# Kernel optimization log

Hardware: AMD Instinct MI355X
Metric: run time of the kernel (lower is better)

## Reference

```python
import jax, jax.numpy as jnp
import numpy as np

B, S, DIM, NH = 256, 64, 1024, 8
DH = DIM // NH
EPS = 1e-6
LN_EPS = 1e-5


def _make_hops(n):
    hops = np.zeros((n, n), dtype=np.int64)
    cur = 1
    for i in range(n):
        for j in range(i + 1, n):
            hops[i, j] = cur
            hops[j, i] = cur
            cur += 1
    return hops, cur


def setup_inputs() -> dict:
    key = jax.random.key(0)
    ks = jax.random.split(key, 8)
    hops_np, curnum = _make_hops(S)
    return {
        "q": jax.random.normal(ks[0], (B, S, DIM), dtype=jnp.float32),
        "k": jax.random.normal(ks[1], (B, S, DIM), dtype=jnp.float32),
        "v": jax.random.normal(ks[2], (B, S, DIM), dtype=jnp.float32),
        "igate_w": jax.random.normal(ks[3], (NH, 3 * DIM), dtype=jnp.float32) * 0.02,
        "igate_b": jax.random.normal(ks[4], (NH,), dtype=jnp.float32) * 0.1,
        "fgate_w": jax.random.normal(ks[5], (NH, 3 * DIM), dtype=jnp.float32) * 0.02,
        "fgate_b": jnp.linspace(3.0, 6.0, NH, dtype=jnp.float32),
        "rpe": jax.random.normal(ks[6], (curnum, DIM), dtype=jnp.float32) * 0.02,
        "ln_w": jax.random.normal(ks[7], (DIM,), dtype=jnp.float32) * 0.1,
        "ln_b": jnp.zeros((DIM,), dtype=jnp.float32),
        "hops": jnp.asarray(hops_np),
    }


def _mlstm_forward(q, k, v, igate_w, igate_b, fgate_w, fgate_b, rpe, ln_w, ln_b, hops):
    Bq, Sq, _ = q.shape
    pos_emb = rpe[hops]                                   # (S, S, DIM)
    gate_in = jnp.concatenate([q, k, v], axis=-1)         # (B, S, 3*DIM)
    ig = gate_in @ igate_w.T + igate_b                    # (B, S, NH)
    fg = gate_in @ fgate_w.T + fgate_b                    # (B, S, NH)
    ig = jnp.transpose(ig, (0, 2, 1))                     # (B, NH, S)
    fg = jnp.transpose(fg, (0, 2, 1))                     # (B, NH, S)

    qh = q.reshape(Bq, Sq, NH, DH).transpose(0, 2, 1, 3)  # (B, NH, S, DH)
    kh = k.reshape(Bq, Sq, NH, DH).transpose(0, 2, 1, 3)
    vh = v.reshape(Bq, Sq, NH, DH).transpose(0, 2, 1, 3)

    # log forget gates, cumulative sum with a leading zero
    log_f = jax.nn.log_sigmoid(fg)                        # (B, NH, S)
    csum = jnp.cumsum(log_f, axis=-1)
    csum = jnp.concatenate([jnp.zeros((Bq, NH, 1), csum.dtype), csum], axis=-1)  # (B,NH,S+1)
    lfm = csum[:, :, :, None] - csum[:, :, None, :]       # (B, NH, S+1, S+1)
    ltr = jnp.tril(jnp.ones((Sq, Sq), dtype=bool))
    log_fg_matrix = jnp.where(ltr, lfm[:, :, 1:, 1:], -jnp.inf)  # (B, NH, S, S)

    log_D = log_fg_matrix + ig[:, :, None, :]             # add i-gate per column
    max_log_D = jnp.max(log_D, axis=-1, keepdims=True)    # rowwise stabilization
    D = jnp.exp(log_D - max_log_D)                        # (B, NH, S, S)

    k_scaled = kh / np.sqrt(DH).astype(np.float32)
    pe = pos_emb.reshape(Sq, Sq, NH, DH)
    k_hop = jnp.einsum('bhvc,vmhc->bhvm', qh, pe)         # (B, NH, S, S)
    qk = jnp.einsum('bhsd,bhtd->bhst', qh, k_scaled)      # (B, NH, S, S)
    C = (qk + k_hop) * D

    normalizer = jnp.maximum(jnp.abs(jnp.sum(C, axis=-1, keepdims=True)), jnp.exp(-max_log_D))
    Cn = C / (normalizer + EPS)
    h = Cn @ vh                                           # (B, NH, S, DH)

    # MultiHeadLayerNorm == group_norm with NH groups: normalize each head over DH
    mu = jnp.mean(h, axis=-1, keepdims=True)
    var = jnp.mean(jnp.square(h - mu), axis=-1, keepdims=True)
    hn = (h - mu) / jnp.sqrt(var + LN_EPS)
    w = (1.0 + ln_w).reshape(NH, DH)                      # residual weight: 1 + w
    b = ln_b.reshape(NH, DH)
    hn = hn * w[None, :, None, :] + b[None, :, None, :]
    return hn.transpose(0, 2, 1, 3).reshape(Bq, Sq, DIM)


def reference(q, k, v, igate_w, igate_b, fgate_w, fgate_b, rpe, ln_w, ln_b, hops):
    return _mlstm_forward(q, k, v, igate_w, igate_b, fgate_w, fgate_b, rpe, ln_w, ln_b, hops)
```

## Files before the change

kernel.cpp:

```cpp
#include <hip/hip_runtime.h>
#include <math.h>

#define BB 256
#define SS 64
#define DIMM 1024
#define NHH 8
#define DHH 128

typedef short bf16x8 __attribute__((ext_vector_type(8)));
typedef float f32x4 __attribute__((ext_vector_type(4)));

__device__ __forceinline__ unsigned f2bf(float f) {
    union { float f; unsigned u; } x{f};
    return (x.u + 0x7FFFu + ((x.u >> 16) & 1u)) >> 16;
}
__device__ __forceinline__ unsigned pk2(float lo, float hi) {
    return f2bf(lo) | (f2bf(hi) << 16);
}
__device__ __forceinline__ float bf2f(unsigned short b) {
    union { unsigned u; float f; } x{((unsigned)b) << 16};
    return x.f;
}
__device__ __forceinline__ void split2(float a, float b, unsigned& hi, unsigned& lo) {
    const unsigned ha = f2bf(a), hb = f2bf(b);
    hi = ha | (hb << 16);
    lo = pk2(a - bf2f((unsigned short)ha), b - bf2f((unsigned short)hb));
}
__device__ __forceinline__ float logsigf(float x) {
    return fminf(x, 0.0f) - log1pf(__expf(-fabsf(x)));
}

__global__ __launch_bounds__(256) void k_gate_mfma(
    const float* __restrict__ q, const float* __restrict__ k, const float* __restrict__ v,
    const float* __restrict__ igw, const float* __restrict__ fgw,
    float* __restrict__ part)
{
    __shared__ unsigned short Xs[64 * 264];
    __shared__ unsigned short Ws[16 * 264];
    const int b = blockIdx.x & 255;
    const int ksl = blockIdx.x >> 8;
    const int t = threadIdx.x;
    const int w = t >> 6, l = t & 63, c = l & 15, g = l >> 4;

    f32x4 acc;
    acc[0] = 0.f; acc[1] = 0.f; acc[2] = 0.f; acc[3] = 0.f;

    for (int step = 0; step < 3; ++step) {
        const int kc = ksl * 3 + step;
        const int tensor = kc >> 2;
        const float* src = (tensor == 0) ? q : (tensor == 1) ? k : v;
        src += ((size_t)b * 64) * 1024 + (kc & 3) * 256;
        {
            const int row = t >> 2, seg = t & 3;
            const float* rp = src + row * 1024;
            #pragma unroll
            for (int e = 0; e < 16; ++e) {
                const int col = e * 16 + seg * 4;
                const float4 x = *reinterpret_cast<const float4*>(rp + col);
                unsigned* dp = reinterpret_cast<unsigned*>(&Xs[row * 264 + col]);
                dp[0] = pk2(x.x, x.y); dp[1] = pk2(x.z, x.w);
            }
        }
        {
            const int o = t >> 4, wseg = t & 15;
            const int p0 = ksl * 768 + step * 256;
            const float* wp = (o < 8 ? igw + o * 3072 : fgw + (o - 8) * 3072) + p0;
            #pragma unroll
            for (int e = 0; e < 4; ++e) {
                const int col = e * 64 + wseg * 4;
                const float4 x = *reinterpret_cast<const float4*>(wp + col);
                unsigned* dp = reinterpret_cast<unsigned*>(&Ws[o * 264 + col]);
                dp[0] = pk2(x.x, x.y); dp[1] = pk2(x.z, x.w);
            }
        }
        __syncthreads();
        #pragma unroll
        for (int kk = 0; kk < 8; ++kk) {
            bf16x8 a  = *reinterpret_cast<const bf16x8*>(&Xs[(16 * w + c) * 264 + 32 * kk + 8 * g]);
            bf16x8 bw = *reinterpret_cast<const bf16x8*>(&Ws[c * 264 + 32 * kk + 8 * g]);
            acc = __builtin_amdgcn_mfma_f32_16x16x32_bf16(a, bw, acc, 0, 0, 0);
        }
        __syncthreads();
    }
    float* pb = part + (((size_t)ksl * 256 + b) * 64) * 16;
    #pragma unroll
    for (int reg = 0; reg < 4; ++reg) {
        const int s = 16 * w + 4 * g + reg;
        pb[s * 16 + c] = acc[reg];
    }
}

__global__ __launch_bounds__(256) void k_gates_final(
    const float* __restrict__ part, const float* __restrict__ igb, const float* __restrict__ fgb,
    float* __restrict__ ig_ws, float* __restrict__ csum_ws, float* __restrict__ pmax_ws)
{
    const int b = blockIdx.x;
    const int t = threadIdx.x;
    __shared__ float red[64][18];
    {
        const int s = t >> 2, oq = t & 3;
        float4 sum = make_float4(0.f, 0.f, 0.f, 0.f);
        #pragma unroll
        for (int ksl = 0; ksl < 4; ++ksl) {
            const float4 p = *reinterpret_cast<const float4*>(
                part + (((size_t)ksl * 256 + b) * 64 + s) * 16 + oq * 4);
            sum.x += p.x; sum.y += p.y; sum.z += p.z; sum.w += p.w;
        }
        red[s][oq * 4 + 0] = sum.x; red[s][oq * 4 + 1] = sum.y;
        red[s][oq * 4 + 2] = sum.z; red[s][oq * 4 + 3] = sum.w;
    }
    __syncthreads();
    if (t < 64) {
        const int s = t;
        #pragma unroll
        for (int h = 0; h < 8; ++h) {
            float ig = red[s][h]     + igb[h];
            float fg = red[s][8 + h] + fgb[h];
            float lf = logsigf(fg);
            float cs = lf;
            #pragma unroll
            for (int d = 1; d < 64; d <<= 1) {
                float o = __shfl_up(cs, (unsigned)d, 64);
                if (s >= d) cs += o;
            }
            float pm = ig - cs;
            #pragma unroll
            for (int d = 1; d < 64; d <<= 1) {
                float o = __shfl_up(pm, (unsigned)d, 64);
                if (s >= d) pm = fmaxf(pm, o);
            }
            const int base = b * NHH + h;
            ig_ws[base * SS + s] = ig;
            csum_ws[base * 65 + s + 1] = cs;
            if (s == 0) csum_ws[base * 65] = 0.0f;
            pmax_ws[base * SS + s] = pm;
        }
    }
}

__global__ __launch_bounds__(256) void k_khop(
    const float* __restrict__ q, const float* __restrict__ rpe, const int* __restrict__ hops,
    float* __restrict__ khop_ws)
{
    __shared__ unsigned short Phi[64 * 136];
    __shared__ unsigned short Plo[64 * 136];
    const int v = blockIdx.x;
    const int h = blockIdx.y;
    const int t = threadIdx.x;
    const int w = t >> 6, l = t & 63, c = l & 15, g = l >> 4;

    const int nelem = (v + 1) * 128;
    for (int idx = t; idx < nelem; idx += 256) {
        const int m = idx >> 7, cc = idx & 127;
        const float x = rpe[(size_t)hops[v * SS + m] * DIMM + h * DHH + cc];
        const unsigned hi = f2bf(x);
        Phi[m * 136 + cc] = (unsigned short)hi;
        Plo[m * 136 + cc] = (unsigned short)f2bf(x - bf2f((unsigned short)hi));
    }
    __syncthreads();

    const int ntiles = (v >> 4) + 1;
    union bfu { unsigned u[4]; bf16x8 vv; };
    #pragma unroll
    for (int ms = 0; ms < 4; ++ms) {
        const int brow = 64 * w + 16 * ms + c;
        const float* qbase = q + ((size_t)brow * SS + v) * DIMM + h * DHH + 8 * g;
        bfu qhi[4], qlo[4];
        #pragma unroll
        for (int kk = 0; kk < 4; ++kk) {
            const float4 f0 = *reinterpret_cast<const float4*>(qbase + 32 * kk);
            const float4 f1 = *reinterpret_cast<const float4*>(qbase + 32 * kk + 4);
            split2(f0.x, f0.y, qhi[kk].u[0], qlo[kk].u[0]);
            split2(f0.z, f0.w, qhi[kk].u[1], qlo[kk].u[1]);
            split2(f1.x, f1.y, qhi[kk].u[2], qlo[kk].u[2]);
            split2(f1.z, f1.w, qhi[kk].u[3], qlo[kk].u[3]);
        }
        for (int n = 0; n < ntiles; ++n) {
            f32x4 acc;
            acc[0] = 0.f; acc[1] = 0.f; acc[2] = 0.f; acc[3] = 0.f;
            #pragma unroll
            for (int kk = 0; kk < 4; ++kk) {
                const int off = (16 * n + c) * 136 + 32 * kk + 8 * g;
                bf16x8 bhi = *reinterpret_cast<const bf16x8*>(&Phi[off]);
                bf16x8 blo = *reinterpret_cast<const bf16x8*>(&Plo[off]);
                acc = __builtin_amdgcn_mfma_f32_16x16x32_bf16(qhi[kk].vv, bhi, acc, 0, 0, 0);
                acc = __builtin_amdgcn_mfma_f32_16x16x32_bf16(qlo[kk].vv, bhi, acc, 0, 0, 0);
                acc = __builtin_amdgcn_mfma_f32_16x16x32_bf16(qhi[kk].vv, blo, acc, 0, 0, 0);
            }
            #pragma unroll
            for (int reg = 0; reg < 4; ++reg) {
                const int bo = 64 * w + 16 * ms + 4 * g + reg;
                khop_ws[(((size_t)bo * NHH + h) * SS + v) * SS + 16 * n + c] = acc[reg];
            }
        }
    }
}

__global__ __launch_bounds__(256) void k_attn(
    const float* __restrict__ q, const float* __restrict__ k, const float* __restrict__ v,
    const float* __restrict__ lnw, const float* __restrict__ lnb,
    const float* __restrict__ ig_ws, const float* __restrict__ csum_ws,
    const float* __restrict__ pmax_ws, const float* __restrict__ khop_ws,
    float* __restrict__ out)
{
    __shared__ __attribute__((aligned(16))) unsigned short Kspl[2 * 64 * 136];
    __shared__ float csum_s[65];
    __shared__ float ig_s[64];
    __shared__ float pmax_s[64];
    __shared__ float lnw_s[128];
    __shared__ float lnb_s[128];

    const int bid = blockIdx.x;
    const int b = bid >> 3, h = bid & 7;
    const int t = threadIdx.x;
    const int w = t >> 6, l = t & 63, c = l & 15, g = l >> 4;
    const float rs_dh = 0.08838834764831845f;

    unsigned short* Khi = Kspl;
    unsigned short* Klo = Kspl + 64 * 136;

    float4 vreg[2][4];
    #pragma unroll
    for (int it = 0; it < 2; ++it) {
        const int u = t + 256 * it;
        const int jp = u >> 4, seg8 = u & 15;
        const float* r0 = v + ((size_t)(b * 64 + 2 * jp)) * 1024 + h * 128 + seg8 * 8;
        vreg[it][0] = *reinterpret_cast<const float4*>(r0);
        vreg[it][1] = *reinterpret_cast<const float4*>(r0 + 4);
        vreg[it][2] = *reinterpret_cast<const float4*>(r0 + 1024);
        vreg[it][3] = *reinterpret_cast<const float4*>(r0 + 1028);
    }

    float kh[4][4];
    {
        const float* khb = khop_ws + ((size_t)(b * NHH + h) * SS) * SS;
        #pragma unroll
        for (int n = 0; n < 4; ++n) {
            #pragma unroll
            for (int reg = 0; reg < 4; ++reg) {
                const int i = 16 * w + 4 * g + reg;
                kh[n][reg] = khb[(size_t)i * SS + 16 * n + c];
            }
        }
    }

    #pragma unroll
    for (int it = 0; it < 2; ++it) {
        const int u = t + 256 * it;
        const int row = u >> 3, seg = u & 7;
        const float* kp = k + ((size_t)(b * 64 + row)) * 1024 + h * 128;
        #pragma unroll
        for (int e = 0; e < 2; ++e) {
            const int col = e * 64 + seg * 8;
            const float4 ya = *reinterpret_cast<const float4*>(kp + col);
            const float4 yb = *reinterpret_cast<const float4*>(kp + col + 4);
            unsigned* dh = reinterpret_cast<unsigned*>(&Khi[row * 136 + col]);
            unsigned* dl = reinterpret_cast<unsigned*>(&Klo[row * 136 + col]);
            split2(ya.x * rs_dh, ya.y * rs_dh, dh[0], dl[0]);
            split2(ya.z * rs_dh, ya.w * rs_dh, dh[1], dl[1]);
            split2(yb.x * rs_dh, yb.y * rs_dh, dh[2], dl[2]);
            split2(yb.z * rs_dh, yb.w * rs_dh, dh[3], dl[3]);
        }
    }
    const int cb = b * NHH + h;
    if (t < 65) csum_s[t] = csum_ws[cb * 65 + t];
    if (t >= 128 && t < 192) ig_s[t - 128] = ig_ws[cb * SS + (t - 128)];
    if (t >= 192) pmax_s[t - 192] = pmax_ws[cb * SS + (t - 192)];
    if (t < 128) lnw_s[t] = lnw[h * 128 + t];
    else if (t < 256) lnb_s[t - 128] = lnb[h * 128 + (t - 128)];

    union bfu { unsigned u[4]; bf16x8 v; };
    bfu qhi[4], qlo[4];
    {
        const int qrow = 16 * w + c;
        const float* qbase = q + ((size_t)(b * 64 + qrow)) * 1024 + h * 128 + 8 * g;
        #pragma unroll
        for (int kk = 0; kk < 4; ++kk) {
            const float4 f0 = *reinterpret_cast<const float4*>(qbase + 32 * kk);
            const float4 f1 = *reinterpret_cast<const float4*>(qbase + 32 * kk + 4);
            split2(f0.x, f0.y, qhi[kk].u[0], qlo[kk].u[0]);
            split2(f0.z, f0.w, qhi[kk].u[1], qlo[kk].u[1]);
            split2(f1.x, f1.y, qhi[kk].u[2], qlo[kk].u[2]);
            split2(f1.z, f1.w, qhi[kk].u[3], qlo[kk].u[3]);
        }
    }
    __syncthreads();

    f32x4 acc[4];
    #pragma unroll
    for (int n = 0; n < 4; ++n) { acc[n][0]=0.f; acc[n][1]=0.f; acc[n][2]=0.f; acc[n][3]=0.f; }
    #pragma unroll
    for (int kk = 0; kk < 4; ++kk) {
        #pragma unroll
        for (int n = 0; n < 4; ++n) {
            const int off = (16 * n + c) * 136 + 32 * kk + 8 * g;
            bf16x8 bhi = *reinterpret_cast<const bf16x8*>(&Khi[off]);
            bf16x8 blo = *reinterpret_cast<const bf16x8*>(&Klo[off]);
            acc[n] = __builtin_amdgcn_mfma_f32_16x16x32_bf16(qhi[kk].v, bhi, acc[n], 0, 0, 0);
            acc[n] = __builtin_amdgcn_mfma_f32_16x16x32_bf16(qlo[kk].v, bhi, acc[n], 0, 0, 0);
            acc[n] = __builtin_amdgcn_mfma_f32_16x16x32_bf16(qhi[kk].v, blo, acc[n], 0, 0, 0);
        }
    }
    __syncthreads();

    unsigned short* VT = Kspl;
    unsigned short* Cn = Kspl + 128 * 72;
    #pragma unroll
    for (int it = 0; it < 2; ++it) {
        const int u = t + 256 * it;
        const int jp = u >> 4, seg8 = u & 15;
        float v0[8], v1[8];
        v0[0]=vreg[it][0].x; v0[1]=vreg[it][0].y; v0[2]=vreg[it][0].z; v0[3]=vreg[it][0].w;
        v0[4]=vreg[it][1].x; v0[5]=vreg[it][1].y; v0[6]=vreg[it][1].z; v0[7]=vreg[it][1].w;
        v1[0]=vreg[it][2].x; v1[1]=vreg[it][2].y; v1[2]=vreg[it][2].z; v1[3]=vreg[it][2].w;
        v1[4]=vreg[it][3].x; v1[5]=vreg[it][3].y; v1[6]=vreg[it][3].z; v1[7]=vreg[it][3].w;
        #pragma unroll
        for (int m = 0; m < 8; ++m) {
            const int cc = seg8 * 8 + m;
            unsigned byte = (unsigned)(cc * 144 + 4 * jp);
            byte ^= ((cc >> 3) & 7) << 4;
            *reinterpret_cast<unsigned*>(reinterpret_cast<char*>(VT) + byte) = pk2(v0[m], v1[m]);
        }
    }

    {
        float mi[4], rs[4];
        #pragma unroll
        for (int reg = 0; reg < 4; ++reg) {
            const int i = 16 * w + 4 * g + reg;
            mi[reg] = csum_s[i + 1] + pmax_s[i];
            rs[reg] = 0.0f;
        }
        #pragma unroll
        for (int n = 0; n < 4; ++n) {
            const int j = 16 * n + c;
            const float cj = csum_s[j + 1], igj = ig_s[j];
            #pragma unroll
            for (int reg = 0; reg < 4; ++reg) {
                const int i = 16 * w + 4 * g + reg;
                float val = 0.0f;
                if (j <= i) {
                    const float sc = acc[n][reg] + kh[n][reg];
                    val = sc * __expf(csum_s[i + 1] - cj + igj - mi[reg]);
                }
                acc[n][reg] = val;
                rs[reg] += val;
            }
        }
        #pragma unroll
        for (int reg = 0; reg < 4; ++reg) {
            float r = rs[reg];
            r += __shfl_xor(r, 1); r += __shfl_xor(r, 2);
            r += __shfl_xor(r, 4); r += __shfl_xor(r, 8);
            const float nrm = fmaxf(fabsf(r), __expf(-mi[reg]));
            const float inv = 1.0f / (nrm + 1e-6f);
            const int i = 16 * w + 4 * g + reg;
            #pragma unroll
            for (int n = 0; n < 4; ++n) {
                const int j = 16 * n + c;
                Cn[i * 72 + j] = (unsigned short)f2bf(acc[n][reg] * inv);
            }
        }
    }
    __syncthreads();

    f32x4 hacc[8];
    #pragma unroll
    for (int n = 0; n < 8; ++n) { hacc[n][0]=0.f; hacc[n][1]=0.f; hacc[n][2]=0.f; hacc[n][3]=0.f; }
    #pragma unroll
    for (int ks = 0; ks < 2; ++ks) {
        bf16x8 a = *reinterpret_cast<const bf16x8*>(&Cn[(16 * w + c) * 72 + 32 * ks + 8 * g]);
        #pragma unroll
        for (int n = 0; n < 8; ++n) {
            const int cc = 16 * n + c;
            unsigned byte = (unsigned)(cc * 144 + 64 * ks + 16 * g);
            byte ^= ((cc >> 3) & 7) << 4;
            bf16x8 bv = *reinterpret_cast<const bf16x8*>(reinterpret_cast<const char*>(VT) + byte);
            hacc[n] = __builtin_amdgcn_mfma_f32_16x16x32_bf16(a, bv, hacc[n], 0, 0, 0);
        }
    }

    #pragma unroll
    for (int reg = 0; reg < 4; ++reg) {
        float s1 = 0.f, s2 = 0.f;
        #pragma unroll
        for (int n = 0; n < 8; ++n) { const float x = hacc[n][reg]; s1 += x; s2 = fmaf(x, x, s2); }
        s1 += __shfl_xor(s1, 1); s1 += __shfl_xor(s1, 2);
        s1 += __shfl_xor(s1, 4); s1 += __shfl_xor(s1, 8);
        s2 += __shfl_xor(s2, 1); s2 += __shfl_xor(s2, 2);
        s2 += __shfl_xor(s2, 4); s2 += __shfl_xor(s2, 8);
        const float mu = s1 * (1.0f / 128.0f);
        const float var = s2 * (1.0f / 128.0f) - mu * mu;
        const float rstd = rsqrtf(var + 1e-5f);
        const int io = 16 * w + 4 * g + reg;
        float* op = out + (((size_t)(b * 64 + io)) * 8 + h) * 128;
        #pragma unroll
        for (int n = 0; n < 8; ++n) {
            const int cc = 16 * n + c;
            op[cc] = (hacc[n][reg] - mu) * rstd * (1.0f + lnw_s[cc]) + lnb_s[cc];
        }
    }
}

extern "C" void kernel_launch(void* const* d_in, const int* in_sizes, int n_in,
                              void* d_out, int out_size, void* d_ws, size_t ws_size,
                              hipStream_t stream) {
    const float* q   = (const float*)d_in[0];
    const float* k   = (const float*)d_in[1];
    const float* v   = (const float*)d_in[2];
    const float* igw = (const float*)d_in[3];
    const float* igb = (const float*)d_in[4];
    const float* fgw = (const float*)d_in[5];
    const float* fgb = (const float*)d_in[6];
    const float* rpe = (const float*)d_in[7];
    const float* lnw = (const float*)d_in[8];
    const float* lnb = (const float*)d_in[9];
    const int*  hops = (const int*)d_in[10];
    float* out = (float*)d_out;

    float* ig_ws   = (float*)d_ws;
    float* pmax_ws = ig_ws + 131072;
    float* csum_ws = pmax_ws + 131072;
    float* part    = csum_ws + 133120;
    float* khop_ws = part;

    hipLaunchKernelGGL(k_gate_mfma, dim3(1024), dim3(256), 0, stream,
                       q, k, v, igw, fgw, part);
    hipLaunchKernelGGL(k_gates_final, dim3(BB), dim3(256), 0, stream,
                       part, igb, fgb, ig_ws, csum_ws, pmax_ws);
    hipLaunchKernelGGL(k_khop, dim3(SS, NHH), dim3(256), 0, stream,
                       q, rpe, hops, khop_ws);
    hipLaunchKernelGGL(k_attn, dim3(BB * NHH), dim3(256), 0, stream,
                       q, k, v, lnw, lnb, ig_ws, csum_ws, pmax_ws, khop_ws, out);
}
```

Measured before the change: 129.0 us.

## Use hardware bf16 pack conversion and skip upper-triangle tiles in causal attention

Replaces the software round-to-nearest bf16 conversion with the v_cvt_pk_bf16_f32 instruction, cutting per-element ALU work in the split and pack helpers. The rpe gather in k_khop now loads float2 pairs and writes packed 32-bit words to shared memory. In the attention kernel each wave skips column tiles above its row block (n > w): the khop loads, QK MFMAs and gating loop for those fully masked tiles are dropped. Skipped accumulators stay zero, which matches the causal mask. The new path adds wave-dependent branching.

```diff
diff --git a/kernel.cpp b/kernel.cpp
--- a/kernel.cpp
+++ b/kernel.cpp
@@ -10,21 +10,24 @@
 typedef short bf16x8 __attribute__((ext_vector_type(8)));
 typedef float f32x4 __attribute__((ext_vector_type(4)));
 
-__device__ __forceinline__ unsigned f2bf(float f) {
-    union { float f; unsigned u; } x{f};
-    return (x.u + 0x7FFFu + ((x.u >> 16) & 1u)) >> 16;
-}
-__device__ __forceinline__ unsigned pk2(float lo, float hi) {
-    return f2bf(lo) | (f2bf(hi) << 16);
+__device__ __forceinline__ unsigned cvtpk(float lo, float hi) {
+    unsigned r;
+    asm("v_cvt_pk_bf16_f32 %0, %1, %2" : "=v"(r) : "v"(lo), "v"(hi));
+    return r;
+}
+__device__ __forceinline__ unsigned pk2(float lo, float hi) { return cvtpk(lo, hi); }
+__device__ __forceinline__ unsigned short f2bh(float x) {
+    return (unsigned short)(cvtpk(x, 0.0f) & 0xFFFFu);
 }
 __device__ __forceinline__ float bf2f(unsigned short b) {
     union { unsigned u; float f; } x{((unsigned)b) << 16};
     return x.f;
 }
 __device__ __forceinline__ void split2(float a, float b, unsigned& hi, unsigned& lo) {
-    const unsigned ha = f2bf(a), hb = f2bf(b);
-    hi = ha | (hb << 16);
-    lo = pk2(a - bf2f((unsigned short)ha), b - bf2f((unsigned short)hb));
+    hi = cvtpk(a, b);
+    const float ha = __uint_as_float(hi << 16);
+    const float hb = __uint_as_float(hi & 0xFFFF0000u);
+    lo = cvtpk(a - ha, b - hb);
 }
 __device__ __forceinline__ float logsigf(float x) {
     return fminf(x, 0.0f) - log1pf(__expf(-fabsf(x)));
@@ -149,13 +152,17 @@
     const int t = threadIdx.x;
     const int w = t >> 6, l = t & 63, c = l & 15, g = l >> 4;
 
-    const int nelem = (v + 1) * 128;
-    for (int idx = t; idx < nelem; idx += 256) {
-        const int m = idx >> 7, cc = idx & 127;
-        const float x = rpe[(size_t)hops[v * SS + m] * DIMM + h * DHH + cc];
-        const unsigned hi = f2bf(x);
-        Phi[m * 136 + cc] = (unsigned short)hi;
-        Plo[m * 136 + cc] = (unsigned short)f2bf(x - bf2f((unsigned short)hi));
+    const int npair = (v + 1) * 64;
+    unsigned* PhiU = reinterpret_cast<unsigned*>(Phi);
+    unsigned* PloU = reinterpret_cast<unsigned*>(Plo);
+    for (int idx = t; idx < npair; idx += 256) {
+        const int m = idx >> 6, cp = idx & 63;
+        const float2 x = *reinterpret_cast<const float2*>(
+            rpe + (size_t)hops[v * SS + m] * DIMM + h * DHH + 2 * cp);
+        unsigned hi, lo;
+        split2(x.x, x.y, hi, lo);
+        PhiU[m * 68 + cp] = hi;
+        PloU[m * 68 + cp] = lo;
     }
     __syncthreads();
 
@@ -236,6 +243,7 @@
         const float* khb = khop_ws + ((size_t)(b * NHH + h) * SS) * SS;
         #pragma unroll
         for (int n = 0; n < 4; ++n) {
+            if (n > w) continue;
             #pragma unroll
             for (int reg = 0; reg < 4; ++reg) {
                 const int i = 16 * w + 4 * g + reg;
@@ -293,6 +301,7 @@
     for (int kk = 0; kk < 4; ++kk) {
         #pragma unroll
         for (int n = 0; n < 4; ++n) {
+            if (n > w) continue;
             const int off = (16 * n + c) * 136 + 32 * kk + 8 * g;
             bf16x8 bhi = *reinterpret_cast<const bf16x8*>(&Khi[off]);
             bf16x8 blo = *reinterpret_cast<const bf16x8*>(&Klo[off]);
@@ -333,6 +342,7 @@
         }
         #pragma unroll
         for (int n = 0; n < 4; ++n) {
+            if (n > w) continue;
             const int j = 16 * n + c;
             const float cj = csum_s[j + 1], igj = ig_s[j];
             #pragma unroll
@@ -358,7 +368,7 @@
             #pragma unroll
             for (int n = 0; n < 4; ++n) {
                 const int j = 16 * n + c;
-                Cn[i * 72 + j] = (unsigned short)f2bf(acc[n][reg] * inv);
+                Cn[i * 72 + j] = f2bh(acc[n][reg] * inv);
             }
         }
     }
```

Result: no change. 129.9 us (+0.7%).
